# Optimization experiments

Hardware: AMD Instinct MI355X
Metric: run time of the kernel (lower is better)

Reference implementation:

```python
import jax, jax.numpy as jnp
import numpy as np

T1, T2 = 10.0, 50.0          # Canny hysteresis thresholds from EdgeNorm
HYST_ITERS = 16              # fixed-iteration approximation of Canny hysteresis BFS
TEMPERATURE = 1.0
NUM_CLASSES_M1 = 13.0


def _shift(a, dy, dx):
    # zero-padded shift of [n,h,w]
    p = jnp.pad(a, ((0, 0), (1, 1), (1, 1)))
    return jax.lax.dynamic_slice(p, (0, 1 + dy, 1 + dx), a.shape)


def _sobel(img):
    # img: [n,h,w] float32; replicate border, aperture-3 Sobel (cv2.Canny default)
    p = jnp.pad(img, ((0, 0), (1, 1), (1, 1)), mode='edge')[:, None]  # [n,1,h+2,w+2]
    kx = jnp.array([[-1, 0, 1], [-2, 0, 2], [-1, 0, 1]], jnp.float32)
    ky = jnp.array([[-1, -2, -1], [0, 0, 0], [1, 2, 1]], jnp.float32)
    k = jnp.stack([kx, ky])[:, None]                                  # [2,1,3,3]
    g = jax.lax.conv_general_dilated(p, k, (1, 1), 'VALID')           # [n,2,h,w]
    return g[:, 0], g[:, 1]


def _canny(img_u8):
    # vectorized Canny over the batch (cv2 loops per sample on CPU)
    img = img_u8.astype(jnp.float32)
    gx, gy = _sobel(img)
    mag = jnp.abs(gx) + jnp.abs(gy)                 # L1 magnitude (cv2 L2gradient=False)
    ang = jnp.mod(jnp.degrees(jnp.arctan2(gy, gx)), 180.0)
    s0 = (ang < 22.5) | (ang >= 157.5)
    s45 = (ang >= 22.5) & (ang < 67.5)
    s90 = (ang >= 67.5) & (ang < 112.5)
    # non-max suppression: compare along quantized gradient direction
    n1 = jnp.where(s0, _shift(mag, 0, 1),
         jnp.where(s45, _shift(mag, -1, 1),
         jnp.where(s90, _shift(mag, -1, 0), _shift(mag, -1, -1))))
    n2 = jnp.where(s0, _shift(mag, 0, -1),
         jnp.where(s45, _shift(mag, 1, -1),
         jnp.where(s90, _shift(mag, 1, 0), _shift(mag, 1, 1))))
    nms = jnp.where((mag >= n1) & (mag >= n2), mag, 0.0)
    strong = nms > T2
    weak = nms > T1

    def body(_, s):
        grown = jax.lax.reduce_window(s.astype(jnp.float32), -jnp.inf, jax.lax.max,
                                      (1, 3, 3), (1, 1, 1),
                                      [(0, 0), (1, 1), (1, 1)]) > 0.0
        return grown & weak

    strong = jax.lax.fori_loop(0, HYST_ITERS, body, strong)
    return strong.astype(jnp.float32) * 255.0       # [n,h,w] in {0,255}


def _dilate_blur(edges):
    # cv2.dilate with 10x10 ones kernel, anchor=(5,5) -> asymmetric (5,4) window pad
    d = jax.lax.reduce_window(edges, -jnp.inf, jax.lax.max,
                              (1, 10, 10), (1, 1, 1),
                              [(0, 0), (5, 4), (5, 4)])
    # cv2.blur 10x10 box filter, reflect101 border, rounded back to uint8
    p = jnp.pad(d, ((0, 0), (5, 4), (5, 4)), mode='reflect')
    b = jax.lax.reduce_window(p, 0.0, jax.lax.add,
                              (1, 10, 10), (1, 1, 1), 'VALID') / 100.0
    return jnp.round(b) / 255.0                     # EdgeNorm: e / 255


def setup_inputs() -> dict:
    key = jax.random.key(0)
    k1, k2 = jax.random.split(key)
    n, c, h, w = 8, 14, 512, 512
    return {
        'preds_S': jax.random.normal(k1, (n, c, h, w), dtype=jnp.float32),
        'preds_T': jax.random.normal(k2, (n, c, h, w), dtype=jnp.float32),
    }


def reference(preds_S, preds_T):
    n, c, h, w = preds_S.shape
    # teacher argmax map -> uint8 grayscale (truncating cast, as torch .type(uint8))
    t_map = (jnp.argmax(preds_T, axis=1).astype(jnp.float32)
             / NUM_CLASSES_M1 * 255.0).astype(jnp.uint8)
    edges = jax.lax.stop_gradient(_dilate_blur(_canny(t_map)))  # [n,h,w], constant wrt grads
    pred_T = edges[:, None] * preds_T
    pred_S = edges[:, None] * preds_S
    # ChannelNorm: softmax over flattened h*w per (n,c); divergence='kl' -> norm_s.log()
    logsm_t = jax.nn.log_softmax(pred_T.reshape(n, c, h * w), axis=-1)
    logsm_s = jax.nn.log_softmax(pred_S.reshape(n, c, h * w), axis=-1)
    norm_t = jnp.exp(logsm_t)
    loss = jnp.sum(norm_t * (logsm_t - logsm_s))    # KLDivLoss(reduction='sum')
    loss = loss / (n * c)                           # channel norm divisor
    return loss * (TEMPERATURE ** 2)
```

## Files before the change

### kernel.cpp

```cpp
#include <hip/hip_runtime.h>
#include <math.h>

#define NB 8
#define CC 14
#define HH 512
#define WW 512
#define HW (HH*WW)
#define NHW (NB*HW)
#define WPR 8
#define WPI (HH*WPR)
#define KSPLIT 32
#define KCHUNK (HW/KSPLIT)

typedef unsigned long long u64;

__global__ __launch_bounds__(256) void k_argmax(const float* __restrict__ T,
                                                uchar4* __restrict__ tmap4) {
    int i4 = blockIdx.x * blockDim.x + threadIdx.x;
    if (i4 >= NHW / 4) return;
    int n  = i4 / (HW / 4);
    int p4 = i4 - n * (HW / 4);
    const float4* base = (const float4*)(T + (size_t)n * CC * HW) + p4;
    float4 best = base[0];
    int b0 = 0, b1 = 0, b2 = 0, b3 = 0;
#pragma unroll
    for (int c = 1; c < CC; ++c) {
        float4 v = base[(size_t)c * (HW / 4)];
        if (v.x > best.x) { best.x = v.x; b0 = c; }
        if (v.y > best.y) { best.y = v.y; b1 = c; }
        if (v.z > best.z) { best.z = v.z; b2 = c; }
        if (v.w > best.w) { best.w = v.w; b3 = c; }
    }
    uchar4 g;
    g.x = (unsigned char)(((float)b0 / 13.0f) * 255.0f);
    g.y = (unsigned char)(((float)b1 / 13.0f) * 255.0f);
    g.z = (unsigned char)(((float)b2 / 13.0f) * 255.0f);
    g.w = (unsigned char)(((float)b3 / 13.0f) * 255.0f);
    tmap4[i4] = g;
}

__global__ __launch_bounds__(256) void k_sobel_nms(const unsigned char* __restrict__ tmap,
                                                   u64* __restrict__ weakBits,
                                                   u64* __restrict__ strongBits) {
    int tx = blockIdx.x, ty = blockIdx.y, n = blockIdx.z;
    int x0 = tx * 64, y0 = ty * 64;
    __shared__ unsigned char tm[68 * 68];
    __shared__ unsigned short ms[66 * 66];
    int tid = threadIdx.x;
    const unsigned char* im = tmap + (size_t)n * HW;

    for (int idx = tid; idx < 68 * 68; idx += 256) {
        int r = idx / 68, c = idx - r * 68;
        int yy = y0 - 2 + r; yy = yy < 0 ? 0 : (yy > HH - 1 ? HH - 1 : yy);
        int xx = x0 - 2 + c; xx = xx < 0 ? 0 : (xx > WW - 1 ? WW - 1 : xx);
        tm[idx] = im[yy * WW + xx];
    }
    __syncthreads();

    for (int idx = tid; idx < 66 * 66; idx += 256) {
        int r = idx / 66, c = idx - r * 66;
        const unsigned char* t0 = tm + r * 68 + c;
        int a00 = t0[0],   a01 = t0[1],   a02 = t0[2];
        int a10 = t0[68],                 a12 = t0[70];
        int a20 = t0[136], a21 = t0[137], a22 = t0[138];
        int gx = (a02 - a00) + 2 * (a12 - a10) + (a22 - a20);
        int gy = (a20 - a00) + 2 * (a21 - a01) + (a22 - a02);
        int m = (gx < 0 ? -gx : gx) + (gy < 0 ? -gy : gy);
        float ang = atan2f((float)gy, (float)gx) * 57.29577951308232f;
        ang = fmodf(ang, 180.0f);
        if (ang < 0.0f) ang += 180.0f;
        int s;
        if (ang < 22.5f || ang >= 157.5f) s = 0;
        else if (ang < 67.5f)             s = 1;
        else if (ang < 112.5f)            s = 2;
        else                              s = 3;
        ms[idx] = (unsigned short)((m << 2) | s);
    }
    __syncthreads();

    int lane = tid & 63;
    int warp = tid >> 6;
#pragma unroll
    for (int it = 0; it < 16; ++it) {
        int row = it * 4 + warp;
        int gy_ = y0 + row, gx_ = x0 + lane;
        int v = ms[(row + 1) * 66 + (lane + 1)];
        int mc = v >> 2, s = v & 3;
        int dy1, dx1, dy2, dx2;
        if (s == 0)      { dy1 = 0;  dx1 = 1;  dy2 = 0; dx2 = -1; }
        else if (s == 1) { dy1 = -1; dx1 = 1;  dy2 = 1; dx2 = -1; }
        else if (s == 2) { dy1 = -1; dx1 = 0;  dy2 = 1; dx2 = 0;  }
        else             { dy1 = -1; dx1 = -1; dy2 = 1; dx2 = 1;  }
        int y1 = gy_ + dy1, x1 = gx_ + dx1, y2 = gy_ + dy2, x2 = gx_ + dx2;
        int n1 = (y1 < 0 || y1 >= HH || x1 < 0 || x1 >= WW)
                 ? 0 : (ms[(row + 1 + dy1) * 66 + (lane + 1 + dx1)] >> 2);
        int n2 = (y2 < 0 || y2 >= HH || x2 < 0 || x2 >= WW)
                 ? 0 : (ms[(row + 1 + dy2) * 66 + (lane + 1 + dx2)] >> 2);
        int nms = (mc >= n1 && mc >= n2) ? mc : 0;
        u64 wm = __ballot(nms > 10);
        u64 sm = __ballot(nms > 50);
        if (lane == 0) {
            size_t w = (size_t)n * WPI + gy_ * WPR + tx;
            weakBits[w]   = wm;
            strongBits[w] = sm;
        }
    }
}

#define TR 32
#define HALO 26
#define TROWS (TR + 2*HALO)
#define TWORDS (TROWS * WPR)
__global__ __launch_bounds__(1024) void k_hyst_dil_blur(const u64* __restrict__ strongBits,
                                                        const u64* __restrict__ weakBits,
                                                        unsigned char* __restrict__ E) {
    int tile = blockIdx.x & 15;
    int n    = blockIdx.x >> 4;
    int t0r  = tile * TR;
    int g0   = t0r - HALO;
    __shared__ u64 A[TWORDS];
    __shared__ u64 B[TWORDS];
    __shared__ u64 Wl[TWORDS];
    __shared__ unsigned char rc[(TR + 10) * 512];
    int tid = threadIdx.x;

    if (tid < TWORDS) {
        int vr = g0 + (tid >> 3);
        int w  = tid & 7;
        u64 sv = 0, wv = 0;
        if (vr >= 0 && vr < HH) {
            sv = strongBits[(size_t)n * WPI + vr * WPR + w];
            wv = weakBits  [(size_t)n * WPI + vr * WPR + w];
        }
        A[tid] = sv;
        Wl[tid] = wv;
    }
    __syncthreads();

#pragma unroll 1
    for (int it = 0; it < 16; ++it) {
        const u64* src = (it & 1) ? B : A;
        u64*       dst = (it & 1) ? A : B;
        if (tid < TWORDS) {
            int r = tid >> 3;
            int w = tid & 7;
            u64 c  = src[tid];
            u64 up = (r > 0)         ? src[tid - 8] : 0;
            u64 dn = (r < TROWS - 1) ? src[tid + 8] : 0;
            u64 a = c | up | dn;
            u64 pL = 0, pR = 0;
            if (w > 0) {
                u64 cl = src[tid - 1];
                u64 ul = (r > 0)         ? src[tid - 9] : 0;
                u64 dl = (r < TROWS - 1) ? src[tid + 7] : 0;
                pL = cl | ul | dl;
            }
            if (w < 7) {
                u64 cr = src[tid + 1];
                u64 ur = (r > 0)         ? src[tid - 7] : 0;
                u64 dr = (r < TROWS - 1) ? src[tid + 9] : 0;
                pR = cr | ur | dr;
            }
            u64 g = a | (a << 1) | (pL >> 63) | (a >> 1) | (pR << 63);
            dst[tid] = g & Wl[tid];
        }
        __syncthreads();
    }

    if (tid < TWORDS) {
        int w = tid & 7;
        u64 v  = A[tid];
        u64 p  = (w > 0) ? A[tid - 1] : 0;
        u64 nx = (w < 7) ? A[tid + 1] : 0;
        u64 o = v;
#pragma unroll
        for (int d = 1; d <= 5; ++d) o |= (v << d) | (p >> (64 - d));
#pragma unroll
        for (int d = 1; d <= 4; ++d) o |= (v >> d) | (nx << (64 - d));
        B[tid] = o;
    }
    __syncthreads();

    u64* D = Wl;
    if (tid < (TR + 10) * WPR) {
        int d = tid >> 3;
        int w = tid & 7;
        int r = d + HALO - 5;
        u64 o = 0;
#pragma unroll
        for (int dy = -5; dy <= 4; ++dy) o |= B[(r + dy) * WPR + w];
        D[d * WPR + w] = o;
    }
    __syncthreads();

    for (int idx = tid; idx < (TR + 10) * 512; idx += 1024) {
        int r = idx >> 9;
        int x = idx & 511;
        int c;
        if (x >= 5 && x <= 507) {
            int b = x - 5, wd = b >> 6, off = b & 63;
            u64 v = D[r * WPR + wd] >> off;
            if (off && wd < 7) v |= D[r * WPR + wd + 1] << (64 - off);
            c = __popcll(v & 0x3FFull);
        } else {
            c = 0;
            for (int dx = -5; dx <= 4; ++dx) {
                int xx = x + dx;
                xx = xx < 0 ? -xx : (xx > WW - 1 ? 2 * (WW - 1) - xx : xx);
                c += (int)((D[r * WPR + (xx >> 6)] >> (xx & 63)) & 1ull);
            }
        }
        rc[idx] = (unsigned char)c;
    }
    __syncthreads();

    for (int idx = tid; idx < TR * 512; idx += 1024) {
        int yy = idx >> 9;
        int x  = idx & 511;
        int gy = t0r + yy;
        int sum = 0;
        if (gy >= 5 && gy <= HH - 5) {
#pragma unroll
            for (int k = 0; k < 10; ++k) sum += rc[(yy + k) * 512 + x];
        } else {
#pragma unroll
            for (int k = 0; k < 10; ++k) {
                int v  = gy - 5 + k;
                int rv = v < 0 ? -v : (v > HH - 1 ? 2 * (HH - 1) - v : v);
                sum += rc[(rv - (t0r - 5)) * 512 + x];
            }
        }
        float b = rintf((255.0f * (float)sum) / 100.0f);
        E[(size_t)n * HW + gy * WW + x] = (unsigned char)b;
    }
}

__global__ __launch_bounds__(256) void k_kl_partial(const float* __restrict__ S,
                                                    const float* __restrict__ T,
                                                    const unsigned char* __restrict__ E,
                                                    double* __restrict__ partial) {
    int cidx  = blockIdx.x;
    int split = blockIdx.y;
    int n = cidx / CC;
    const float4* Tp = (const float4*)(T + (size_t)cidx * HW + (size_t)split * KCHUNK);
    const float4* Sp = (const float4*)(S + (size_t)cidx * HW + (size_t)split * KCHUNK);
    const uchar4* Ep = (const uchar4*)(E + (size_t)n    * HW + (size_t)split * KCHUNK);
    int tid = threadIdx.x;

    float Zt = 0.0f, Wt = 0.0f, Zs = 0.0f;
#pragma unroll
    for (int k = 0; k < KCHUNK / 4 / 256; ++k) {
        int j = k * 256 + tid;
        float4 t4 = Tp[j];
        float4 s4 = Sp[j];
        uchar4 e4 = Ep[j];
#pragma unroll
        for (int u = 0; u < 4; ++u) {
            float e = (float)((&e4.x)[u]) / 255.0f;
            float t = e * (&t4.x)[u];
            float s = e * (&s4.x)[u];
            float et = __expf(t);
            Zt += et;
            Wt += et * (t - s);
            Zs += __expf(s);
        }
    }

    double zt = (double)Zt, wt = (double)Wt, zs = (double)Zs;
#pragma unroll
    for (int off = 32; off > 0; off >>= 1) {
        zt += __shfl_down(zt, off);
        wt += __shfl_down(wt, off);
        zs += __shfl_down(zs, off);
    }
    __shared__ double wr[4][3];
    int wv = tid >> 6, ln = tid & 63;
    if (ln == 0) { wr[wv][0] = zt; wr[wv][1] = wt; wr[wv][2] = zs; }
    __syncthreads();
    if (tid == 0) {
        double* o = partial + ((size_t)cidx * KSPLIT + split) * 3;
        o[0] = wr[0][0] + wr[1][0] + wr[2][0] + wr[3][0];
        o[1] = wr[0][1] + wr[1][1] + wr[2][1] + wr[3][1];
        o[2] = wr[0][2] + wr[1][2] + wr[2][2] + wr[3][2];
    }
}

__global__ __launch_bounds__(128) void k_kl_final(const double* __restrict__ partial,
                                                  float* __restrict__ out) {
    int tid = threadIdx.x;
    double loss = 0.0;
    if (tid < NB * CC) {
        double Zt = 0.0, Wt = 0.0, Zs = 0.0;
        for (int sp = 0; sp < KSPLIT; ++sp) {
            const double* p = partial + ((size_t)tid * KSPLIT + sp) * 3;
            Zt += p[0]; Wt += p[1]; Zs += p[2];
        }
        loss = Wt / Zt - log(Zt) + log(Zs);
    }
    __shared__ double red[128];
    red[tid] = loss;
    __syncthreads();
    for (int off = 64; off > 0; off >>= 1) {
        if (tid < off) red[tid] += red[tid + off];
        __syncthreads();
    }
    if (tid == 0) out[0] = (float)(red[0] / (double)(NB * CC));
}

extern "C" void kernel_launch(void* const* d_in, const int* in_sizes, int n_in,
                              void* d_out, int out_size, void* d_ws, size_t ws_size,
                              hipStream_t stream) {
    const float* S = (const float*)d_in[0];
    const float* T = (const float*)d_in[1];
    float* out = (float*)d_out;

    char* ws = (char*)d_ws;
    unsigned char* e_buf      = (unsigned char*)(ws);
    unsigned char* tmap       = (unsigned char*)(ws + (size_t)NHW);
    u64*           weakBits   = (u64*)(ws + (size_t)NHW * 2);
    u64*           strongBits = (u64*)(ws + (size_t)NHW * 2 + (NHW/8));
    double*        partial    = (double*)(ws + (size_t)NHW * 2 + 2*(NHW/8));

    k_argmax<<<dim3(NHW / 4 / 256), dim3(256), 0, stream>>>(T, (uchar4*)tmap);
    k_sobel_nms<<<dim3(8, 8, NB), dim3(256), 0, stream>>>(tmap, weakBits, strongBits);
    k_hyst_dil_blur<<<dim3(NB * 16), dim3(1024), 0, stream>>>(strongBits, weakBits, e_buf);
    k_kl_partial<<<dim3(NB * CC, KSPLIT), dim3(256), 0, stream>>>(S, T, e_buf, partial);
    k_kl_final<<<1, 128, 0, stream>>>(partial, out);
    (void)in_sizes; (void)n_in; (void)out_size; (void)ws_size;
}
```

Measured before the change: 288.1 us.

## Fuse all stages into one cooperative persistent kernel with grid syncs

Replaces the five separate kernel launches with a single cooperative kernel of 512 blocks that runs argmax, Sobel/NMS, hysteresis+dilate+blur and the KL partial/final reductions as phases separated by grid.sync(). The hysteresis tile height is halved so 256 blocks cover the images, and all stages share one reused shared-memory buffer. The goal is to remove launch gaps and inter-kernel drain/fill. In exchange, phases now run at fixed block counts with 256 threads per block, and grid-wide barriers add cost. Halving the tile height also raises the share of halo rows recomputed in hysteresis.

Result: slower. 514.5 us (+78.6%).

```diff
diff --git a/kernel.cpp b/kernel.cpp
--- a/kernel.cpp
+++ b/kernel.cpp
@@ -1,5 +1,8 @@
 #include <hip/hip_runtime.h>
+#include <hip/hip_cooperative_groups.h>
 #include <math.h>
+
+namespace cg = cooperative_groups;
 
 #define NB 8
 #define CC 14
@@ -12,299 +15,323 @@
 #define KSPLIT 32
 #define KCHUNK (HW/KSPLIT)
 
-typedef unsigned long long u64;
-
-__global__ __launch_bounds__(256) void k_argmax(const float* __restrict__ T,
-                                                uchar4* __restrict__ tmap4) {
-    int i4 = blockIdx.x * blockDim.x + threadIdx.x;
-    if (i4 >= NHW / 4) return;
-    int n  = i4 / (HW / 4);
-    int p4 = i4 - n * (HW / 4);
-    const float4* base = (const float4*)(T + (size_t)n * CC * HW) + p4;
-    float4 best = base[0];
-    int b0 = 0, b1 = 0, b2 = 0, b3 = 0;
-#pragma unroll
-    for (int c = 1; c < CC; ++c) {
-        float4 v = base[(size_t)c * (HW / 4)];
-        if (v.x > best.x) { best.x = v.x; b0 = c; }
-        if (v.y > best.y) { best.y = v.y; b1 = c; }
-        if (v.z > best.z) { best.z = v.z; b2 = c; }
-        if (v.w > best.w) { best.w = v.w; b3 = c; }
-    }
-    uchar4 g;
-    g.x = (unsigned char)(((float)b0 / 13.0f) * 255.0f);
-    g.y = (unsigned char)(((float)b1 / 13.0f) * 255.0f);
-    g.z = (unsigned char)(((float)b2 / 13.0f) * 255.0f);
-    g.w = (unsigned char)(((float)b3 / 13.0f) * 255.0f);
-    tmap4[i4] = g;
-}
-
-__global__ __launch_bounds__(256) void k_sobel_nms(const unsigned char* __restrict__ tmap,
-                                                   u64* __restrict__ weakBits,
-                                                   u64* __restrict__ strongBits) {
-    int tx = blockIdx.x, ty = blockIdx.y, n = blockIdx.z;
-    int x0 = tx * 64, y0 = ty * 64;
-    __shared__ unsigned char tm[68 * 68];
-    __shared__ unsigned short ms[66 * 66];
-    int tid = threadIdx.x;
-    const unsigned char* im = tmap + (size_t)n * HW;
-
-    for (int idx = tid; idx < 68 * 68; idx += 256) {
-        int r = idx / 68, c = idx - r * 68;
-        int yy = y0 - 2 + r; yy = yy < 0 ? 0 : (yy > HH - 1 ? HH - 1 : yy);
-        int xx = x0 - 2 + c; xx = xx < 0 ? 0 : (xx > WW - 1 ? WW - 1 : xx);
-        tm[idx] = im[yy * WW + xx];
-    }
-    __syncthreads();
-
-    for (int idx = tid; idx < 66 * 66; idx += 256) {
-        int r = idx / 66, c = idx - r * 66;
-        const unsigned char* t0 = tm + r * 68 + c;
-        int a00 = t0[0],   a01 = t0[1],   a02 = t0[2];
-        int a10 = t0[68],                 a12 = t0[70];
-        int a20 = t0[136], a21 = t0[137], a22 = t0[138];
-        int gx = (a02 - a00) + 2 * (a12 - a10) + (a22 - a20);
-        int gy = (a20 - a00) + 2 * (a21 - a01) + (a22 - a02);
-        int m = (gx < 0 ? -gx : gx) + (gy < 0 ? -gy : gy);
-        float ang = atan2f((float)gy, (float)gx) * 57.29577951308232f;
-        ang = fmodf(ang, 180.0f);
-        if (ang < 0.0f) ang += 180.0f;
-        int s;
-        if (ang < 22.5f || ang >= 157.5f) s = 0;
-        else if (ang < 67.5f)             s = 1;
-        else if (ang < 112.5f)            s = 2;
-        else                              s = 3;
-        ms[idx] = (unsigned short)((m << 2) | s);
-    }
-    __syncthreads();
-
-    int lane = tid & 63;
-    int warp = tid >> 6;
-#pragma unroll
-    for (int it = 0; it < 16; ++it) {
-        int row = it * 4 + warp;
-        int gy_ = y0 + row, gx_ = x0 + lane;
-        int v = ms[(row + 1) * 66 + (lane + 1)];
-        int mc = v >> 2, s = v & 3;
-        int dy1, dx1, dy2, dx2;
-        if (s == 0)      { dy1 = 0;  dx1 = 1;  dy2 = 0; dx2 = -1; }
-        else if (s == 1) { dy1 = -1; dx1 = 1;  dy2 = 1; dx2 = -1; }
-        else if (s == 2) { dy1 = -1; dx1 = 0;  dy2 = 1; dx2 = 0;  }
-        else             { dy1 = -1; dx1 = -1; dy2 = 1; dx2 = 1;  }
-        int y1 = gy_ + dy1, x1 = gx_ + dx1, y2 = gy_ + dy2, x2 = gx_ + dx2;
-        int n1 = (y1 < 0 || y1 >= HH || x1 < 0 || x1 >= WW)
-                 ? 0 : (ms[(row + 1 + dy1) * 66 + (lane + 1 + dx1)] >> 2);
-        int n2 = (y2 < 0 || y2 >= HH || x2 < 0 || x2 >= WW)
-                 ? 0 : (ms[(row + 1 + dy2) * 66 + (lane + 1 + dx2)] >> 2);
-        int nms = (mc >= n1 && mc >= n2) ? mc : 0;
-        u64 wm = __ballot(nms > 10);
-        u64 sm = __ballot(nms > 50);
-        if (lane == 0) {
-            size_t w = (size_t)n * WPI + gy_ * WPR + tx;
-            weakBits[w]   = wm;
-            strongBits[w] = sm;
-        }
-    }
-}
-
-#define TR 32
+#define GRID 512
+#define BLK  256
+
+#define TR 16
 #define HALO 26
 #define TROWS (TR + 2*HALO)
 #define TWORDS (TROWS * WPR)
-__global__ __launch_bounds__(1024) void k_hyst_dil_blur(const u64* __restrict__ strongBits,
-                                                        const u64* __restrict__ weakBits,
-                                                        unsigned char* __restrict__ E) {
-    int tile = blockIdx.x & 15;
-    int n    = blockIdx.x >> 4;
-    int t0r  = tile * TR;
-    int g0   = t0r - HALO;
-    __shared__ u64 A[TWORDS];
-    __shared__ u64 B[TWORDS];
-    __shared__ u64 Wl[TWORDS];
-    __shared__ unsigned char rc[(TR + 10) * 512];
-    int tid = threadIdx.x;
-
-    if (tid < TWORDS) {
-        int vr = g0 + (tid >> 3);
-        int w  = tid & 7;
-        u64 sv = 0, wv = 0;
-        if (vr >= 0 && vr < HH) {
-            sv = strongBits[(size_t)n * WPI + vr * WPR + w];
-            wv = weakBits  [(size_t)n * WPI + vr * WPR + w];
-        }
-        A[tid] = sv;
-        Wl[tid] = wv;
-    }
-    __syncthreads();
+#define DROWS (TR + 10)
+#define DWORDS (DROWS * WPR)
+
+typedef unsigned long long u64;
+
+#define SMEM_U64 3296
+
+__global__ __launch_bounds__(BLK, 2) void k_mega(
+    const float* __restrict__ S, const float* __restrict__ T,
+    unsigned char* __restrict__ tmap,
+    u64* __restrict__ weakBits, u64* __restrict__ strongBits,
+    unsigned char* __restrict__ E,
+    double* __restrict__ partial, float* __restrict__ out)
+{
+    cg::grid_group grid = cg::this_grid();
+    __shared__ u64 smem[SMEM_U64];
+    const int b   = blockIdx.x;
+    const int tid = threadIdx.x;
+
+    {
+        uchar4* tmap4 = (uchar4*)tmap;
+        int gt = b * BLK + tid;
+#pragma unroll
+        for (int q = 0; q < 4; ++q) {
+            int i4 = gt + q * (GRID * BLK);
+            int n  = i4 / (HW / 4);
+            int p4 = i4 - n * (HW / 4);
+            const float4* base = (const float4*)(T + (size_t)n * CC * HW) + p4;
+            float4 best = base[0];
+            int b0 = 0, b1 = 0, b2 = 0, b3 = 0;
+#pragma unroll
+            for (int c = 1; c < CC; ++c) {
+                float4 v = base[(size_t)c * (HW / 4)];
+                if (v.x > best.x) { best.x = v.x; b0 = c; }
+                if (v.y > best.y) { best.y = v.y; b1 = c; }
+                if (v.z > best.z) { best.z = v.z; b2 = c; }
+                if (v.w > best.w) { best.w = v.w; b3 = c; }
+            }
+            uchar4 g;
+            g.x = (unsigned char)(((float)b0 / 13.0f) * 255.0f);
+            g.y = (unsigned char)(((float)b1 / 13.0f) * 255.0f);
+            g.z = (unsigned char)(((float)b2 / 13.0f) * 255.0f);
+            g.w = (unsigned char)(((float)b3 / 13.0f) * 255.0f);
+            tmap4[i4] = g;
+        }
+    }
+    grid.sync();
+
+    {
+        int n  = b >> 6;
+        int ty = (b >> 3) & 7;
+        int tx = b & 7;
+        int x0 = tx * 64, y0 = ty * 64;
+        unsigned char*  tm = (unsigned char*)smem;
+        unsigned short* ms = (unsigned short*)((char*)smem + 4624);
+        const unsigned char* im = tmap + (size_t)n * HW;
+
+        for (int idx = tid; idx < 68 * 68; idx += BLK) {
+            int r = idx / 68, c = idx - r * 68;
+            int yy = y0 - 2 + r; yy = yy < 0 ? 0 : (yy > HH - 1 ? HH - 1 : yy);
+            int xx = x0 - 2 + c; xx = xx < 0 ? 0 : (xx > WW - 1 ? WW - 1 : xx);
+            tm[idx] = im[yy * WW + xx];
+        }
+        __syncthreads();
+
+        for (int idx = tid; idx < 66 * 66; idx += BLK) {
+            int r = idx / 66, c = idx - r * 66;
+            const unsigned char* t0 = tm + r * 68 + c;
+            int a00 = t0[0],   a01 = t0[1],   a02 = t0[2];
+            int a10 = t0[68],                 a12 = t0[70];
+            int a20 = t0[136], a21 = t0[137], a22 = t0[138];
+            int gx = (a02 - a00) + 2 * (a12 - a10) + (a22 - a20);
+            int gy = (a20 - a00) + 2 * (a21 - a01) + (a22 - a02);
+            int m = (gx < 0 ? -gx : gx) + (gy < 0 ? -gy : gy);
+            float ang = atan2f((float)gy, (float)gx) * 57.29577951308232f;
+            ang = fmodf(ang, 180.0f);
+            if (ang < 0.0f) ang += 180.0f;
+            int s;
+            if (ang < 22.5f || ang >= 157.5f) s = 0;
+            else if (ang < 67.5f)             s = 1;
+            else if (ang < 112.5f)            s = 2;
+            else                              s = 3;
+            ms[idx] = (unsigned short)((m << 2) | s);
+        }
+        __syncthreads();
+
+        int lane = tid & 63;
+        int warp = tid >> 6;
+#pragma unroll
+        for (int it = 0; it < 16; ++it) {
+            int row = it * 4 + warp;
+            int gy_ = y0 + row, gx_ = x0 + lane;
+            int v = ms[(row + 1) * 66 + (lane + 1)];
+            int mc = v >> 2, s = v & 3;
+            int dy1, dx1, dy2, dx2;
+            if (s == 0)      { dy1 = 0;  dx1 = 1;  dy2 = 0; dx2 = -1; }
+            else if (s == 1) { dy1 = -1; dx1 = 1;  dy2 = 1; dx2 = -1; }
+            else if (s == 2) { dy1 = -1; dx1 = 0;  dy2 = 1; dx2 = 0;  }
+            else             { dy1 = -1; dx1 = -1; dy2 = 1; dx2 = 1;  }
+            int y1 = gy_ + dy1, x1 = gx_ + dx1, y2 = gy_ + dy2, x2 = gx_ + dx2;
+            int n1 = (y1 < 0 || y1 >= HH || x1 < 0 || x1 >= WW)
+                     ? 0 : (ms[(row + 1 + dy1) * 66 + (lane + 1 + dx1)] >> 2);
+            int n2 = (y2 < 0 || y2 >= HH || x2 < 0 || x2 >= WW)
+                     ? 0 : (ms[(row + 1 + dy2) * 66 + (lane + 1 + dx2)] >> 2);
+            int nms = (mc >= n1 && mc >= n2) ? mc : 0;
+            u64 wm = __ballot(nms > 10);
+            u64 sm = __ballot(nms > 50);
+            if (lane == 0) {
+                size_t w = (size_t)n * WPI + gy_ * WPR + tx;
+                weakBits[w]   = wm;
+                strongBits[w] = sm;
+            }
+        }
+        __syncthreads();
+    }
+    grid.sync();
+
+    if (b < NB * 32) {
+        int n    = b >> 5;
+        int tile = b & 31;
+        int t0r  = tile * TR;
+        int g0   = t0r - HALO;
+        u64* A  = smem;
+        u64* Bb = smem + TWORDS;
+        u64* Wl = smem + 2 * TWORDS;
+        unsigned char* rc = (unsigned char*)(smem + 3 * TWORDS);
+
+        for (int i = tid; i < TWORDS; i += BLK) {
+            int vr = g0 + (i >> 3);
+            int w  = i & 7;
+            u64 sv = 0, wv = 0;
+            if (vr >= 0 && vr < HH) {
+                sv = strongBits[(size_t)n * WPI + vr * WPR + w];
+                wv = weakBits  [(size_t)n * WPI + vr * WPR + w];
+            }
+            A[i] = sv;
+            Wl[i] = wv;
+        }
+        __syncthreads();
 
 #pragma unroll 1
-    for (int it = 0; it < 16; ++it) {
-        const u64* src = (it & 1) ? B : A;
-        u64*       dst = (it & 1) ? A : B;
-        if (tid < TWORDS) {
-            int r = tid >> 3;
-            int w = tid & 7;
-            u64 c  = src[tid];
-            u64 up = (r > 0)         ? src[tid - 8] : 0;
-            u64 dn = (r < TROWS - 1) ? src[tid + 8] : 0;
-            u64 a = c | up | dn;
-            u64 pL = 0, pR = 0;
-            if (w > 0) {
-                u64 cl = src[tid - 1];
-                u64 ul = (r > 0)         ? src[tid - 9] : 0;
-                u64 dl = (r < TROWS - 1) ? src[tid + 7] : 0;
-                pL = cl | ul | dl;
-            }
-            if (w < 7) {
-                u64 cr = src[tid + 1];
-                u64 ur = (r > 0)         ? src[tid - 7] : 0;
-                u64 dr = (r < TROWS - 1) ? src[tid + 9] : 0;
-                pR = cr | ur | dr;
-            }
-            u64 g = a | (a << 1) | (pL >> 63) | (a >> 1) | (pR << 63);
-            dst[tid] = g & Wl[tid];
-        }
-        __syncthreads();
-    }
-
-    if (tid < TWORDS) {
-        int w = tid & 7;
-        u64 v  = A[tid];
-        u64 p  = (w > 0) ? A[tid - 1] : 0;
-        u64 nx = (w < 7) ? A[tid + 1] : 0;
-        u64 o = v;
-#pragma unroll
-        for (int d = 1; d <= 5; ++d) o |= (v << d) | (p >> (64 - d));
-#pragma unroll
-        for (int d = 1; d <= 4; ++d) o |= (v >> d) | (nx << (64 - d));
-        B[tid] = o;
-    }
-    __syncthreads();
-
-    u64* D = Wl;
-    if (tid < (TR + 10) * WPR) {
-        int d = tid >> 3;
-        int w = tid & 7;
-        int r = d + HALO - 5;
-        u64 o = 0;
-#pragma unroll
-        for (int dy = -5; dy <= 4; ++dy) o |= B[(r + dy) * WPR + w];
-        D[d * WPR + w] = o;
-    }
-    __syncthreads();
-
-    for (int idx = tid; idx < (TR + 10) * 512; idx += 1024) {
-        int r = idx >> 9;
-        int x = idx & 511;
-        int c;
-        if (x >= 5 && x <= 507) {
-            int b = x - 5, wd = b >> 6, off = b & 63;
-            u64 v = D[r * WPR + wd] >> off;
-            if (off && wd < 7) v |= D[r * WPR + wd + 1] << (64 - off);
-            c = __popcll(v & 0x3FFull);
-        } else {
-            c = 0;
-            for (int dx = -5; dx <= 4; ++dx) {
-                int xx = x + dx;
-                xx = xx < 0 ? -xx : (xx > WW - 1 ? 2 * (WW - 1) - xx : xx);
-                c += (int)((D[r * WPR + (xx >> 6)] >> (xx & 63)) & 1ull);
-            }
-        }
-        rc[idx] = (unsigned char)c;
-    }
-    __syncthreads();
-
-    for (int idx = tid; idx < TR * 512; idx += 1024) {
-        int yy = idx >> 9;
-        int x  = idx & 511;
-        int gy = t0r + yy;
-        int sum = 0;
-        if (gy >= 5 && gy <= HH - 5) {
-#pragma unroll
-            for (int k = 0; k < 10; ++k) sum += rc[(yy + k) * 512 + x];
-        } else {
-#pragma unroll
-            for (int k = 0; k < 10; ++k) {
-                int v  = gy - 5 + k;
-                int rv = v < 0 ? -v : (v > HH - 1 ? 2 * (HH - 1) - v : v);
-                sum += rc[(rv - (t0r - 5)) * 512 + x];
-            }
-        }
-        float b = rintf((255.0f * (float)sum) / 100.0f);
-        E[(size_t)n * HW + gy * WW + x] = (unsigned char)b;
-    }
-}
-
-__global__ __launch_bounds__(256) void k_kl_partial(const float* __restrict__ S,
-                                                    const float* __restrict__ T,
-                                                    const unsigned char* __restrict__ E,
-                                                    double* __restrict__ partial) {
-    int cidx  = blockIdx.x;
-    int split = blockIdx.y;
-    int n = cidx / CC;
-    const float4* Tp = (const float4*)(T + (size_t)cidx * HW + (size_t)split * KCHUNK);
-    const float4* Sp = (const float4*)(S + (size_t)cidx * HW + (size_t)split * KCHUNK);
-    const uchar4* Ep = (const uchar4*)(E + (size_t)n    * HW + (size_t)split * KCHUNK);
-    int tid = threadIdx.x;
-
-    float Zt = 0.0f, Wt = 0.0f, Zs = 0.0f;
-#pragma unroll
-    for (int k = 0; k < KCHUNK / 4 / 256; ++k) {
-        int j = k * 256 + tid;
-        float4 t4 = Tp[j];
-        float4 s4 = Sp[j];
-        uchar4 e4 = Ep[j];
-#pragma unroll
-        for (int u = 0; u < 4; ++u) {
-            float e = (float)((&e4.x)[u]) / 255.0f;
-            float t = e * (&t4.x)[u];
-            float s = e * (&s4.x)[u];
-            float et = __expf(t);
-            Zt += et;
-            Wt += et * (t - s);
-            Zs += __expf(s);
-        }
-    }
-
-    double zt = (double)Zt, wt = (double)Wt, zs = (double)Zs;
-#pragma unroll
-    for (int off = 32; off > 0; off >>= 1) {
-        zt += __shfl_down(zt, off);
-        wt += __shfl_down(wt, off);
-        zs += __shfl_down(zs, off);
-    }
-    __shared__ double wr[4][3];
-    int wv = tid >> 6, ln = tid & 63;
-    if (ln == 0) { wr[wv][0] = zt; wr[wv][1] = wt; wr[wv][2] = zs; }
-    __syncthreads();
-    if (tid == 0) {
-        double* o = partial + ((size_t)cidx * KSPLIT + split) * 3;
-        o[0] = wr[0][0] + wr[1][0] + wr[2][0] + wr[3][0];
-        o[1] = wr[0][1] + wr[1][1] + wr[2][1] + wr[3][1];
-        o[2] = wr[0][2] + wr[1][2] + wr[2][2] + wr[3][2];
-    }
-}
-
-__global__ __launch_bounds__(128) void k_kl_final(const double* __restrict__ partial,
-                                                  float* __restrict__ out) {
-    int tid = threadIdx.x;
-    double loss = 0.0;
-    if (tid < NB * CC) {
-        double Zt = 0.0, Wt = 0.0, Zs = 0.0;
-        for (int sp = 0; sp < KSPLIT; ++sp) {
-            const double* p = partial + ((size_t)tid * KSPLIT + sp) * 3;
-            Zt += p[0]; Wt += p[1]; Zs += p[2];
-        }
-        loss = Wt / Zt - log(Zt) + log(Zs);
-    }
-    __shared__ double red[128];
-    red[tid] = loss;
-    __syncthreads();
-    for (int off = 64; off > 0; off >>= 1) {
-        if (tid < off) red[tid] += red[tid + off];
-        __syncthreads();
-    }
-    if (tid == 0) out[0] = (float)(red[0] / (double)(NB * CC));
+        for (int it = 0; it < 16; ++it) {
+            const u64* src = (it & 1) ? Bb : A;
+            u64*       dst = (it & 1) ? A : Bb;
+            for (int i = tid; i < TWORDS; i += BLK) {
+                int r = i >> 3;
+                int w = i & 7;
+                u64 c  = src[i];
+                u64 up = (r > 0)         ? src[i - 8] : 0;
+                u64 dn = (r < TROWS - 1) ? src[i + 8] : 0;
+                u64 a = c | up | dn;
+                u64 pL = 0, pR = 0;
+                if (w > 0) {
+                    u64 cl = src[i - 1];
+                    u64 ul = (r > 0)         ? src[i - 9] : 0;
+                    u64 dl = (r < TROWS - 1) ? src[i + 7] : 0;
+                    pL = cl | ul | dl;
+                }
+                if (w < 7) {
+                    u64 cr = src[i + 1];
+                    u64 ur = (r > 0)         ? src[i - 7] : 0;
+                    u64 dr = (r < TROWS - 1) ? src[i + 9] : 0;
+                    pR = cr | ur | dr;
+                }
+                u64 g = a | (a << 1) | (pL >> 63) | (a >> 1) | (pR << 63);
+                dst[i] = g & Wl[i];
+            }
+            __syncthreads();
+        }
+
+        for (int i = tid; i < TWORDS; i += BLK) {
+            int w = i & 7;
+            u64 v  = A[i];
+            u64 p  = (w > 0) ? A[i - 1] : 0;
+            u64 nx = (w < 7) ? A[i + 1] : 0;
+            u64 o = v;
+#pragma unroll
+            for (int d = 1; d <= 5; ++d) o |= (v << d) | (p >> (64 - d));
+#pragma unroll
+            for (int d = 1; d <= 4; ++d) o |= (v >> d) | (nx << (64 - d));
+            Bb[i] = o;
+        }
+        __syncthreads();
+
+        u64* D = Wl;
+        for (int i = tid; i < DWORDS; i += BLK) {
+            int d = i >> 3;
+            int w = i & 7;
+            int r = d + HALO - 5;
+            u64 o = 0;
+#pragma unroll
+            for (int dy = -5; dy <= 4; ++dy) o |= Bb[(r + dy) * WPR + w];
+            D[d * WPR + w] = o;
+        }
+        __syncthreads();
+
+        for (int idx = tid; idx < DROWS * 512; idx += BLK) {
+            int r = idx >> 9;
+            int x = idx & 511;
+            int c;
+            if (x >= 5 && x <= 507) {
+                int bo = x - 5, wd = bo >> 6, off = bo & 63;
+                u64 v = D[r * WPR + wd] >> off;
+                if (off && wd < 7) v |= D[r * WPR + wd + 1] << (64 - off);
+                c = __popcll(v & 0x3FFull);
+            } else {
+                c = 0;
+                for (int dx = -5; dx <= 4; ++dx) {
+                    int xx = x + dx;
+                    xx = xx < 0 ? -xx : (xx > WW - 1 ? 2 * (WW - 1) - xx : xx);
+                    c += (int)((D[r * WPR + (xx >> 6)] >> (xx & 63)) & 1ull);
+                }
+            }
+            rc[idx] = (unsigned char)c;
+        }
+        __syncthreads();
+
+        for (int idx = tid; idx < TR * 512; idx += BLK) {
+            int yy = idx >> 9;
+            int x  = idx & 511;
+            int gy = t0r + yy;
+            int sum = 0;
+            if (gy >= 5 && gy <= HH - 5) {
+#pragma unroll
+                for (int k = 0; k < 10; ++k) sum += rc[(yy + k) * 512 + x];
+            } else {
+#pragma unroll
+                for (int k = 0; k < 10; ++k) {
+                    int v  = gy - 5 + k;
+                    int rv = v < 0 ? -v : (v > HH - 1 ? 2 * (HH - 1) - v : v);
+                    sum += rc[(rv - (t0r - 5)) * 512 + x];
+                }
+            }
+            float bb = rintf((255.0f * (float)sum) / 100.0f);
+            E[(size_t)n * HW + gy * WW + x] = (unsigned char)bb;
+        }
+    }
+    grid.sync();
+
+    {
+        double* wr = (double*)smem;
+#pragma unroll 1
+        for (int q = 0; q < 7; ++q) {
+            int tk    = b + q * GRID;
+            int cidx  = tk >> 5;
+            int split = tk & 31;
+            int n = cidx / CC;
+            const float4* Tp = (const float4*)(T + (size_t)cidx * HW + (size_t)split * KCHUNK);
+            const float4* Sp = (const float4*)(S + (size_t)cidx * HW + (size_t)split * KCHUNK);
+            const uchar4* Ep = (const uchar4*)(E + (size_t)n    * HW + (size_t)split * KCHUNK);
+
+            float Zt = 0.0f, Wt = 0.0f, Zs = 0.0f;
+#pragma unroll
+            for (int k = 0; k < KCHUNK / 4 / BLK; ++k) {
+                int j = k * BLK + tid;
+                float4 t4 = Tp[j];
+                float4 s4 = Sp[j];
+                uchar4 e4 = Ep[j];
+#pragma unroll
+                for (int u = 0; u < 4; ++u) {
+                    float e = (float)((&e4.x)[u]) / 255.0f;
+                    float t = e * (&t4.x)[u];
+                    float s = e * (&s4.x)[u];
+                    float et = __expf(t);
+                    Zt += et;
+                    Wt += et * (t - s);
+                    Zs += __expf(s);
+                }
+            }
+
+            double zt = (double)Zt, wt = (double)Wt, zs = (double)Zs;
+#pragma unroll
+            for (int off = 32; off > 0; off >>= 1) {
+                zt += __shfl_down(zt, off);
+                wt += __shfl_down(wt, off);
+                zs += __shfl_down(zs, off);
+            }
+            int wv = tid >> 6, ln = tid & 63;
+            __syncthreads();
+            if (ln == 0) { wr[wv * 3 + 0] = zt; wr[wv * 3 + 1] = wt; wr[wv * 3 + 2] = zs; }
+            __syncthreads();
+            if (tid == 0) {
+                double* o = partial + ((size_t)cidx * KSPLIT + split) * 3;
+                o[0] = wr[0] + wr[3] + wr[6] + wr[9];
+                o[1] = wr[1] + wr[4] + wr[7] + wr[10];
+                o[2] = wr[2] + wr[5] + wr[8] + wr[11];
+            }
+        }
+    }
+    grid.sync();
+
+    if (b == 0) {
+        double loss = 0.0;
+        if (tid < NB * CC) {
+            double Zt = 0.0, Wt = 0.0, Zs = 0.0;
+            for (int sp = 0; sp < KSPLIT; ++sp) {
+                const double* p = partial + ((size_t)tid * KSPLIT + sp) * 3;
+                Zt += p[0]; Wt += p[1]; Zs += p[2];
+            }
+            loss = Wt / Zt - log(Zt) + log(Zs);
+        }
+        double* red = (double*)smem;
+        red[tid] = (tid < 128) ? loss : 0.0;
+        __syncthreads();
+        for (int off = 128; off > 0; off >>= 1) {
+            if (tid < off) red[tid] += red[tid + off];
+            __syncthreads();
+        }
+        if (tid == 0) out[0] = (float)(red[0] / (double)(NB * CC));
+    }
 }
 
 extern "C" void kernel_launch(void* const* d_in, const int* in_sizes, int n_in,
@@ -321,10 +348,8 @@
     u64*           strongBits = (u64*)(ws + (size_t)NHW * 2 + (NHW/8));
     double*        partial    = (double*)(ws + (size_t)NHW * 2 + 2*(NHW/8));
 
-    k_argmax<<<dim3(NHW / 4 / 256), dim3(256), 0, stream>>>(T, (uchar4*)tmap);
-    k_sobel_nms<<<dim3(8, 8, NB), dim3(256), 0, stream>>>(tmap, weakBits, strongBits);
-    k_hyst_dil_blur<<<dim3(NB * 16), dim3(1024), 0, stream>>>(strongBits, weakBits, e_buf);
-    k_kl_partial<<<dim3(NB * CC, KSPLIT), dim3(256), 0, stream>>>(S, T, e_buf, partial);
-    k_kl_final<<<1, 128, 0, stream>>>(partial, out);
+    void* args[] = { (void*)&S, (void*)&T, (void*)&tmap, (void*)&weakBits,
+                     (void*)&strongBits, (void*)&e_buf, (void*)&partial, (void*)&out };
+    hipLaunchCooperativeKernel((void*)k_mega, dim3(GRID), dim3(BLK), args, 0, stream);
     (void)in_sizes; (void)n_in; (void)out_size; (void)ws_size;
 }
```
